# Kernel optimization log

Measured on AMD Instinct MI355X. Metric: run time of the kernel, lower is better.

The kernel has to match this reference:

```python
import jax, jax.numpy as jnp
import numpy as np

N_NODES = 100000
N_EDGES = 800000
IN_FEATS = 128
HIDDEN = 64
SCALE = 0.5 ** 0.5  # sqrt(0.5) residual scale
BN_EPS = 1e-5


def setup_inputs() -> dict:
    key = jax.random.key(0)
    ks = jax.random.split(key, 12)
    return {
        "src": jax.random.randint(ks[0], (N_EDGES,), 0, N_NODES, dtype=jnp.int64)
        if jax.config.jax_enable_x64 else jax.random.randint(ks[0], (N_EDGES,), 0, N_NODES),
        "dst": jax.random.randint(ks[1], (N_EDGES,), 0, N_NODES),
        "x": jax.random.normal(ks[2], (N_NODES, IN_FEATS), dtype=jnp.float32),
        "fc_w": jax.random.normal(ks[3], (IN_FEATS, HIDDEN), dtype=jnp.float32) * 0.05,
        "fc_b": jax.random.normal(ks[4], (HIDDEN,), dtype=jnp.float32) * 0.05,
        "w1": jax.random.normal(ks[5], (HIDDEN, HIDDEN), dtype=jnp.float32) * 0.05,
        "b1": jax.random.normal(ks[6], (HIDDEN,), dtype=jnp.float32) * 0.05,
        "w2": jax.random.normal(ks[7], (HIDDEN, HIDDEN), dtype=jnp.float32) * 0.05,
        "b2": jax.random.normal(ks[8], (HIDDEN,), dtype=jnp.float32) * 0.05,
        "gamma": jax.random.normal(ks[9], (HIDDEN,), dtype=jnp.float32) * 0.05 + 1.0,
        "beta": jax.random.normal(ks[10], (HIDDEN,), dtype=jnp.float32) * 0.05,
    }


def _graph_conv(h, w, b, src, dst, norm_src, norm_dst, n_nodes):
    # DGL GraphConv, norm='both': y = D_in^{-1/2} A D_out^{-1/2} (h W) + b
    h = h @ w                                   # [N, H]
    m = h[src] * norm_src[:, None]              # gather + src-degree norm, [E, H]
    agg = jax.ops.segment_sum(m, dst, num_segments=n_nodes)  # scatter-add, [N, H]
    return agg * norm_dst[:, None] + b


def reference(src, dst, x, fc_w, fc_b, w1, b1, w2, b2, gamma, beta):
    n_nodes = x.shape[0]
    ones_e = jnp.ones(src.shape[0], dtype=x.dtype)
    deg_out = jnp.clip(jax.ops.segment_sum(ones_e, src, num_segments=n_nodes), 1.0)
    deg_in = jnp.clip(jax.ops.segment_sum(ones_e, dst, num_segments=n_nodes), 1.0)
    norm_src = (deg_out ** -0.5)[src]           # per-edge source normalization
    norm_dst = deg_in ** -0.5                   # per-node destination normalization

    h = x @ fc_w + fc_b                          # fc: [N, H]
    h = (h + _graph_conv(h, w1, b1, src, dst, norm_src, norm_dst, n_nodes)) * SCALE
    h = (h + _graph_conv(h, w2, b2, src, dst, norm_src, norm_dst, n_nodes)) * SCALE

    # BatchNorm1d (training-mode batch statistics over nodes, biased variance)
    mu = h.mean(axis=0)
    var = ((h - mu) ** 2).mean(axis=0)
    h = (h - mu) * jax.lax.rsqrt(var + BN_EPS) * gamma + beta
    return h
```

## Files before the change

kernel.cpp:

```cpp
#include <hip/hip_runtime.h>

#define HIDDEN 64
#define INFEAT 128
#define SCALE_C 0.70710678118654752f
#define BN_EPS 1e-5f
#define AGG_GRID 2048
#define RED_BLK 32

__device__ __forceinline__ void hist_body(int bid, const int* __restrict__ src,
    const int* __restrict__ dst, int* __restrict__ degO, int* __restrict__ degI, int E){
  int e = bid * 256 + threadIdx.x;
  if (e < E){
    atomicAdd(&degO[src[e]], 1);
    atomicAdd(&degI[dst[e]], 1);
  }
}

__device__ __forceinline__ void place_body(int bid, const int* __restrict__ src,
    const int* __restrict__ dst, int* __restrict__ cur, int* __restrict__ cs, int E){
  int e = bid * 256 + threadIdx.x;
  if (e < E){
    int pos = atomicAdd(&cur[dst[e]], 1);
    cs[pos] = src[e];
  }
}

template<int KDIM, bool ADDB, bool SCALEROW>
__device__ __forceinline__ void gemm_body(int bid, const float* __restrict__ X,
    const float* __restrict__ W, const float* __restrict__ B,
    float* __restrict__ Y, const float* __restrict__ nrm, int N)
{
  __shared__ float xl[128 * 33];
  const int tid  = threadIdx.x;
  const int lane = tid & 63;
  const int wid  = __builtin_amdgcn_readfirstlane(tid >> 6);
  const int nodehalf = wid >> 1;
  const int c0 = (wid & 1) * 32;
  const int base = bid * 128;
  const int myNode = nodehalf * 64 + lane;
  const int gnode = base + myNode;

  float acc[32];
  #pragma unroll
  for (int c = 0; c < 32; ++c) acc[c] = ADDB ? B[c0 + c] : 0.f;

  constexpr int NCHUNK = KDIM / 32;
  #pragma unroll 1
  for (int ck = 0; ck < NCHUNK; ++ck){
    __syncthreads();
    #pragma unroll
    for (int i = 0; i < 4; ++i){
      int f  = i * 256 + tid;
      int nd = f >> 3;
      int kq = f & 7;
      float4 v = make_float4(0.f, 0.f, 0.f, 0.f);
      if (base + nd < N)
        v = *(const float4*)(X + (size_t)(base + nd) * KDIM + ck * 32 + kq * 4);
      float* p = &xl[nd * 33 + kq * 4];
      p[0] = v.x; p[1] = v.y; p[2] = v.z; p[3] = v.w;
    }
    __syncthreads();
    const float* wrow = W + (size_t)ck * 32 * HIDDEN + c0;
    #pragma unroll
    for (int k = 0; k < 32; ++k){
      float xv = xl[myNode * 33 + k];
      #pragma unroll
      for (int c = 0; c < 32; ++c)
        acc[c] = fmaf(xv, wrow[k * HIDDEN + c], acc[c]);
    }
  }

  if (gnode < N){
    float sc = SCALEROW ? nrm[gnode] : 1.f;
    float4* yp = (float4*)(Y + (size_t)gnode * HIDDEN + c0);
    #pragma unroll
    for (int j = 0; j < 8; ++j)
      yp[j] = make_float4(acc[4*j]*sc, acc[4*j+1]*sc, acc[4*j+2]*sc, acc[4*j+3]*sc);
  }
}

__device__ __forceinline__ int role_gemm_idx(int b, int GB, int TOT, int& histIdx){
  int fb  = (int)(((long)b * GB) / TOT);
  int fb1 = (int)(((long)(b + 1) * GB) / TOT);
  histIdx = b - fb;
  return (fb1 > fb) ? fb : -1;
}

__global__ __launch_bounds__(256) void k_mega1(const int* __restrict__ src,
    const int* __restrict__ dst, int* __restrict__ degO, int* __restrict__ degI, int E,
    const float* __restrict__ x, const float* __restrict__ fc_w,
    const float* __restrict__ fc_b, float* __restrict__ h, int N, int GB, int TOT){
  int hIdx;
  int g = role_gemm_idx(blockIdx.x, GB, TOT, hIdx);
  if (g >= 0) gemm_body<INFEAT, true, false>(g, x, fc_w, fc_b, h, nullptr, N);
  else        hist_body(hIdx, src, dst, degO, degI, E);
}

__global__ __launch_bounds__(256) void k_mega2(const int* __restrict__ src,
    const int* __restrict__ dst, int* __restrict__ cur, int* __restrict__ cs, int E,
    const float* __restrict__ h, const float* __restrict__ w1,
    float* __restrict__ t, const float* __restrict__ norm_out, int N, int GB, int TOT){
  int hIdx;
  int g = role_gemm_idx(blockIdx.x, GB, TOT, hIdx);
  if (g >= 0) gemm_body<HIDDEN, false, true>(g, h, w1, nullptr, t, norm_out, N);
  else        place_body(hIdx, src, dst, cur, cs, E);
}

__global__ __launch_bounds__(256) void k_gemm64(const float* __restrict__ X,
    const float* __restrict__ W, float* __restrict__ Y,
    const float* __restrict__ nrm, int N){
  gemm_body<HIDDEN, false, true>(blockIdx.x, X, W, nullptr, Y, nrm, N);
}

__global__ void k_scan1(const int* __restrict__ deg, int* __restrict__ bsum, int N){
  __shared__ int sh[256];
  int t = threadIdx.x;
  int i = blockIdx.x * 256 + t;
  sh[t] = (i < N) ? deg[i] : 0;
  __syncthreads();
  for (int ofs = 128; ofs > 0; ofs >>= 1){
    if (t < ofs) sh[t] += sh[t + ofs];
    __syncthreads();
  }
  if (t == 0) bsum[blockIdx.x] = sh[0];
}

__global__ void k_scan2(int* __restrict__ bsum, int NB){
  __shared__ int sh[512];
  int t = threadIdx.x;
  int v = (t < NB) ? bsum[t] : 0;
  sh[t] = v;
  __syncthreads();
  for (int ofs = 1; ofs < 512; ofs <<= 1){
    int u = (t >= ofs) ? sh[t - ofs] : 0;
    __syncthreads();
    sh[t] += u;
    __syncthreads();
  }
  if (t < NB) bsum[t] = sh[t] - v;
}

__global__ void k_scan3(const int* __restrict__ degI, const int* __restrict__ degO,
                        const int* __restrict__ bofs, int* __restrict__ rp,
                        int* __restrict__ cur, float* __restrict__ norm_out,
                        float* __restrict__ norm_in, int N, int E){
  __shared__ int sh[256];
  int t = threadIdx.x;
  int i = blockIdx.x * 256 + t;
  int v = (i < N) ? degI[i] : 0;
  sh[t] = v;
  __syncthreads();
  for (int ofs = 1; ofs < 256; ofs <<= 1){
    int u = (t >= ofs) ? sh[t - ofs] : 0;
    __syncthreads();
    sh[t] += u;
    __syncthreads();
  }
  if (i < N){
    int excl = sh[t] - v + bofs[blockIdx.x];
    rp[i] = excl; cur[i] = excl;
    if (i == N - 1) rp[N] = E;
    norm_out[i] = rsqrtf((float)max(degO[i], 1));
    norm_in[i]  = rsqrtf((float)max(v, 1));
  }
}

template<bool BN>
__global__ __launch_bounds__(256) void k_agg(const int* __restrict__ rp, const int* __restrict__ cs,
    const float* __restrict__ t, const float* __restrict__ norm_in,
    const float* __restrict__ b, float* __restrict__ h, float* __restrict__ bnpart, int N)
{
  const int tid = threadIdx.x;
  const int lane = tid & 63;
  const int wv = (blockIdx.x * 256 + tid) >> 6;
  const int nw = (gridDim.x * 256) >> 6;
  const float bv = b[lane];
  float s1 = 0.f, s2 = 0.f;

  for (int n = wv; n < N; n += nw){
    const int start = rp[n], end = rp[n + 1];
    float acc = 0.f;
    for (int j0 = start; j0 < end; j0 += 64){
      int cnt = end - j0; if (cnt > 64) cnt = 64;
      int sidx = (j0 + lane < end) ? cs[j0 + lane] : 0;
      int d = 0;
      for (; d + 4 <= cnt; d += 4){
        int a0 = __shfl(sidx, d),     a1 = __shfl(sidx, d + 1);
        int a2 = __shfl(sidx, d + 2), a3 = __shfl(sidx, d + 3);
        float v0 = t[(size_t)a0 * HIDDEN + lane];
        float v1 = t[(size_t)a1 * HIDDEN + lane];
        float v2 = t[(size_t)a2 * HIDDEN + lane];
        float v3 = t[(size_t)a3 * HIDDEN + lane];
        acc += v0; acc += v1; acc += v2; acc += v3;
      }
      for (; d < cnt; ++d){
        int a0 = __shfl(sidx, d);
        acc += t[(size_t)a0 * HIDDEN + lane];
      }
    }
    size_t idx = (size_t)n * HIDDEN + lane;
    float v = (h[idx] + acc * norm_in[n] + bv) * SCALE_C;
    h[idx] = v;
    if (BN){ s1 += v; s2 += v * v; }
  }

  if (BN){
    __shared__ float l1[256], l2[256];
    l1[tid] = s1; l2[tid] = s2;
    __syncthreads();
    if (tid < 64){
      float a1 = l1[tid] + l1[tid+64] + l1[tid+128] + l1[tid+192];
      float a2 = l2[tid] + l2[tid+64] + l2[tid+128] + l2[tid+192];
      bnpart[blockIdx.x * 128 + tid] = a1;
      bnpart[blockIdx.x * 128 + 64 + tid] = a2;
    }
  }
}

__global__ __launch_bounds__(256) void k_bnred(const float* __restrict__ bnpart,
    float* __restrict__ bnred, int nblk){
  int col  = threadIdx.x & 127;
  int half = threadIdx.x >> 7;
  int rows = nblk / RED_BLK;
  int r0 = blockIdx.x * rows;
  float s = 0.f;
  for (int r = half; r < rows; r += 2)
    s += bnpart[(size_t)(r0 + r) * 128 + col];
  __shared__ float sh[256];
  sh[threadIdx.x] = s;
  __syncthreads();
  if (threadIdx.x < 128)
    bnred[blockIdx.x * 128 + threadIdx.x] = sh[threadIdx.x] + sh[threadIdx.x + 128];
}

__global__ void k_bnfin(const float* __restrict__ bnred,
    const float* __restrict__ gamma, const float* __restrict__ beta,
    float* __restrict__ bnab, float invN){
  int c = threadIdx.x;
  float s1 = 0.f, s2 = 0.f;
  #pragma unroll
  for (int b = 0; b < RED_BLK; ++b){ s1 += bnred[b*128 + c]; s2 += bnred[b*128 + 64 + c]; }
  float mu  = s1 * invN;
  float var = s2 * invN - mu * mu;
  float rstd = rsqrtf(var + BN_EPS);
  float sc = gamma[c] * rstd;
  bnab[c] = sc;
  bnab[64 + c] = beta[c] - mu * sc;
}

__global__ void k_bnapply(float* __restrict__ h, const float* __restrict__ bnab, long total4){
  long i = (long)blockIdx.x * blockDim.x + threadIdx.x;
  if (i < total4){
    int c = (int)((i * 4) & 63);
    float4 v = ((float4*)h)[i];
    v.x = fmaf(v.x, bnab[c],     bnab[64 + c]);
    v.y = fmaf(v.y, bnab[c + 1], bnab[65 + c]);
    v.z = fmaf(v.z, bnab[c + 2], bnab[66 + c]);
    v.w = fmaf(v.w, bnab[c + 3], bnab[67 + c]);
    ((float4*)h)[i] = v;
  }
}

extern "C" void kernel_launch(void* const* d_in, const int* in_sizes, int n_in,
                              void* d_out, int out_size, void* d_ws, size_t ws_size,
                              hipStream_t stream){
  const int* src = (const int*)d_in[0];
  const int* dst = (const int*)d_in[1];
  const float* x     = (const float*)d_in[2];
  const float* fc_w  = (const float*)d_in[3];
  const float* fc_b  = (const float*)d_in[4];
  const float* w1    = (const float*)d_in[5];
  const float* b1    = (const float*)d_in[6];
  const float* w2    = (const float*)d_in[7];
  const float* b2    = (const float*)d_in[8];
  const float* gamma = (const float*)d_in[9];
  const float* beta  = (const float*)d_in[10];
  const int E = in_sizes[0];
  const int N = in_sizes[2] / INFEAT;
  const int NB = (N + 255) / 256;
  const int EB = (E + 255) / 256;
  const int GB = (N + 127) / 128;
  const int TOT = EB + GB;

  float* h = (float*)d_out;

  float* t        = (float*)d_ws;
  float* norm_out = t + (size_t)N * HIDDEN;
  float* norm_in  = norm_out + N;
  float* bnpart   = norm_in + N;
  float* bnred    = bnpart + AGG_GRID * 128;
  float* bnab     = bnred + RED_BLK * 128;
  int*   degO     = (int*)(bnab + 128);
  int*   degI     = degO + N;
  int*   rp       = degI + N;
  int*   cur      = rp + N + 1;
  int*   bsum     = cur + N;
  int*   cs       = bsum + 512;

  hipMemsetAsync(degO, 0, 2 * (size_t)N * sizeof(int), stream);

  k_mega1<<<TOT, 256, 0, stream>>>(src, dst, degO, degI, E,
                                   x, fc_w, fc_b, h, N, GB, TOT);

  k_scan1<<<NB, 256, 0, stream>>>(degI, bsum, N);
  k_scan2<<<1, 512, 0, stream>>>(bsum, NB);
  k_scan3<<<NB, 256, 0, stream>>>(degI, degO, bsum, rp, cur, norm_out, norm_in, N, E);

  k_mega2<<<TOT, 256, 0, stream>>>(src, dst, cur, cs, E,
                                   h, w1, t, norm_out, N, GB, TOT);

  k_agg<false><<<AGG_GRID, 256, 0, stream>>>(rp, cs, t, norm_in, b1, h, nullptr, N);

  k_gemm64<<<GB, 256, 0, stream>>>(h, w2, t, norm_out, N);
  k_agg<true><<<AGG_GRID, 256, 0, stream>>>(rp, cs, t, norm_in, b2, h, bnpart, N);

  k_bnred<<<RED_BLK, 256, 0, stream>>>(bnpart, bnred, AGG_GRID);
  k_bnfin<<<1, 64, 0, stream>>>(bnred, gamma, beta, bnab, 1.0f / (float)N);
  long total4 = (long)N * HIDDEN / 4;
  k_bnapply<<<(int)((total4 + 255) / 256), 256, 0, stream>>>(h, bnab, total4);
}
```

Before: 384.3 us.

## Fuse second GEMM into first aggregation epilogue using register-held W2

Folds the layer-2 feature transform (h @ w2 scaled by norm_out) into the layer-1 aggregation kernel. Each wavefront keeps its column of w2 in 64 registers and broadcasts the freshly computed row with readlane. This removes one kernel launch and one full re-read of h. The gather loop also switches from shfl to readlane and unrolls to 8 loads in flight. In exchange it adds register pressure that may lower occupancy of the latency-bound gather, and a second N×64 workspace buffer.

Result: slower. 410.7 us (+6.9%).

```diff
diff --git a/kernel.cpp b/kernel.cpp
--- a/kernel.cpp
+++ b/kernel.cpp
@@ -6,6 +6,11 @@
 #define BN_EPS 1e-5f
 #define AGG_GRID 2048
 #define RED_BLK 32
+
+__device__ __forceinline__ int rli(int v, int l){ return __builtin_amdgcn_readlane(v, l); }
+__device__ __forceinline__ float rlf(float v, int l){
+  return __uint_as_float(__builtin_amdgcn_readlane(__float_as_uint(v), l));
+}
 
 __device__ __forceinline__ void hist_body(int bid, const int* __restrict__ src,
     const int* __restrict__ dst, int* __restrict__ degO, int* __restrict__ degI, int E){
@@ -106,12 +111,6 @@
   else        place_body(hIdx, src, dst, cur, cs, E);
 }
 
-__global__ __launch_bounds__(256) void k_gemm64(const float* __restrict__ X,
-    const float* __restrict__ W, float* __restrict__ Y,
-    const float* __restrict__ nrm, int N){
-  gemm_body<HIDDEN, false, true>(blockIdx.x, X, W, nullptr, Y, nrm, N);
-}
-
 __global__ void k_scan1(const int* __restrict__ deg, int* __restrict__ bsum, int N){
   __shared__ int sh[256];
   int t = threadIdx.x;
@@ -165,10 +164,71 @@
   }
 }
 
-template<bool BN>
-__global__ __launch_bounds__(256) void k_agg(const int* __restrict__ rp, const int* __restrict__ cs,
-    const float* __restrict__ t, const float* __restrict__ norm_in,
-    const float* __restrict__ b, float* __restrict__ h, float* __restrict__ bnpart, int N)
+__device__ __forceinline__ float gather_row(const int* __restrict__ rp,
+    const int* __restrict__ cs, const float* __restrict__ t, int n, int lane){
+  const int start = rp[n], end = rp[n + 1];
+  float acc = 0.f;
+  for (int j0 = start; j0 < end; j0 += 64){
+    int cnt = end - j0; if (cnt > 64) cnt = 64;
+    int sidx = (j0 + lane < end) ? cs[j0 + lane] : 0;
+    int d = 0;
+    for (; d + 8 <= cnt; d += 8){
+      int a0 = rli(sidx, d),   a1 = rli(sidx, d+1);
+      int a2 = rli(sidx, d+2), a3 = rli(sidx, d+3);
+      int a4 = rli(sidx, d+4), a5 = rli(sidx, d+5);
+      int a6 = rli(sidx, d+6), a7 = rli(sidx, d+7);
+      float v0 = t[(size_t)a0 * HIDDEN + lane];
+      float v1 = t[(size_t)a1 * HIDDEN + lane];
+      float v2 = t[(size_t)a2 * HIDDEN + lane];
+      float v3 = t[(size_t)a3 * HIDDEN + lane];
+      float v4 = t[(size_t)a4 * HIDDEN + lane];
+      float v5 = t[(size_t)a5 * HIDDEN + lane];
+      float v6 = t[(size_t)a6 * HIDDEN + lane];
+      float v7 = t[(size_t)a7 * HIDDEN + lane];
+      acc += v0; acc += v1; acc += v2; acc += v3;
+      acc += v4; acc += v5; acc += v6; acc += v7;
+    }
+    for (; d < cnt; ++d)
+      acc += t[(size_t)rli(sidx, d) * HIDDEN + lane];
+  }
+  return acc;
+}
+
+__global__ __launch_bounds__(256) void k_aggmv(const int* __restrict__ rp,
+    const int* __restrict__ cs, const float* __restrict__ t1,
+    const float* __restrict__ norm_in, const float* __restrict__ norm_out,
+    const float* __restrict__ b, const float* __restrict__ w2,
+    float* __restrict__ h, float* __restrict__ t2, int N)
+{
+  const int tid = threadIdx.x;
+  const int lane = tid & 63;
+  const int wv = (blockIdx.x * 256 + tid) >> 6;
+  const int nw = (gridDim.x * 256) >> 6;
+  const float bv = b[lane];
+
+  float w2r[64];
+  #pragma unroll
+  for (int k = 0; k < 64; ++k) w2r[k] = w2[k * HIDDEN + lane];
+
+  for (int n = wv; n < N; n += nw){
+    float acc = gather_row(rp, cs, t1, n, lane);
+    size_t idx = (size_t)n * HIDDEN + lane;
+    float v = (h[idx] + acc * norm_in[n] + bv) * SCALE_C;
+    h[idx] = v;
+    float ta = 0.f, tb = 0.f;
+    #pragma unroll
+    for (int k = 0; k < 64; k += 2){
+      ta = fmaf(rlf(v, k),     w2r[k],     ta);
+      tb = fmaf(rlf(v, k + 1), w2r[k + 1], tb);
+    }
+    t2[idx] = (ta + tb) * norm_out[n];
+  }
+}
+
+__global__ __launch_bounds__(256) void k_agg2(const int* __restrict__ rp,
+    const int* __restrict__ cs, const float* __restrict__ t2,
+    const float* __restrict__ norm_in, const float* __restrict__ b,
+    float* __restrict__ h, float* __restrict__ bnpart, int N)
 {
   const int tid = threadIdx.x;
   const int lane = tid & 63;
@@ -178,42 +238,21 @@
   float s1 = 0.f, s2 = 0.f;
 
   for (int n = wv; n < N; n += nw){
-    const int start = rp[n], end = rp[n + 1];
-    float acc = 0.f;
-    for (int j0 = start; j0 < end; j0 += 64){
-      int cnt = end - j0; if (cnt > 64) cnt = 64;
-      int sidx = (j0 + lane < end) ? cs[j0 + lane] : 0;
-      int d = 0;
-      for (; d + 4 <= cnt; d += 4){
-        int a0 = __shfl(sidx, d),     a1 = __shfl(sidx, d + 1);
-        int a2 = __shfl(sidx, d + 2), a3 = __shfl(sidx, d + 3);
-        float v0 = t[(size_t)a0 * HIDDEN + lane];
-        float v1 = t[(size_t)a1 * HIDDEN + lane];
-        float v2 = t[(size_t)a2 * HIDDEN + lane];
-        float v3 = t[(size_t)a3 * HIDDEN + lane];
-        acc += v0; acc += v1; acc += v2; acc += v3;
-      }
-      for (; d < cnt; ++d){
-        int a0 = __shfl(sidx, d);
-        acc += t[(size_t)a0 * HIDDEN + lane];
-      }
-    }
+    float acc = gather_row(rp, cs, t2, n, lane);
     size_t idx = (size_t)n * HIDDEN + lane;
     float v = (h[idx] + acc * norm_in[n] + bv) * SCALE_C;
     h[idx] = v;
-    if (BN){ s1 += v; s2 += v * v; }
-  }
-
-  if (BN){
-    __shared__ float l1[256], l2[256];
-    l1[tid] = s1; l2[tid] = s2;
-    __syncthreads();
-    if (tid < 64){
-      float a1 = l1[tid] + l1[tid+64] + l1[tid+128] + l1[tid+192];
-      float a2 = l2[tid] + l2[tid+64] + l2[tid+128] + l2[tid+192];
-      bnpart[blockIdx.x * 128 + tid] = a1;
-      bnpart[blockIdx.x * 128 + 64 + tid] = a2;
-    }
+    s1 += v; s2 += v * v;
+  }
+
+  __shared__ float l1[256], l2[256];
+  l1[tid] = s1; l2[tid] = s2;
+  __syncthreads();
+  if (tid < 64){
+    float a1 = l1[tid] + l1[tid+64] + l1[tid+128] + l1[tid+192];
+    float a2 = l2[tid] + l2[tid+64] + l2[tid+128] + l2[tid+192];
+    bnpart[blockIdx.x * 128 + tid] = a1;
+    bnpart[blockIdx.x * 128 + 64 + tid] = a2;
   }
 }
 
@@ -284,8 +323,9 @@
 
   float* h = (float*)d_out;
 
-  float* t        = (float*)d_ws;
-  float* norm_out = t + (size_t)N * HIDDEN;
+  float* t1       = (float*)d_ws;
+  float* t2       = t1 + (size_t)N * HIDDEN;
+  float* norm_out = t2 + (size_t)N * HIDDEN;
   float* norm_in  = norm_out + N;
   float* bnpart   = norm_in + N;
   float* bnred    = bnpart + AGG_GRID * 128;
@@ -307,12 +347,11 @@
   k_scan3<<<NB, 256, 0, stream>>>(degI, degO, bsum, rp, cur, norm_out, norm_in, N, E);
 
   k_mega2<<<TOT, 256, 0, stream>>>(src, dst, cur, cs, E,
-                                   h, w1, t, norm_out, N, GB, TOT);
-
-  k_agg<false><<<AGG_GRID, 256, 0, stream>>>(rp, cs, t, norm_in, b1, h, nullptr, N);
-
-  k_gemm64<<<GB, 256, 0, stream>>>(h, w2, t, norm_out, N);
-  k_agg<true><<<AGG_GRID, 256, 0, stream>>>(rp, cs, t, norm_in, b2, h, bnpart, N);
+                                   h, w1, t1, norm_out, N, GB, TOT);
+
+  k_aggmv<<<AGG_GRID, 256, 0, stream>>>(rp, cs, t1, norm_in, norm_out, b1, w2, h, t2, N);
+
+  k_agg2<<<AGG_GRID, 256, 0, stream>>>(rp, cs, t2, norm_in, b2, h, bnpart, N);
 
   k_bnred<<<RED_BLK, 256, 0, stream>>>(bnpart, bnred, AGG_GRID);
   k_bnfin<<<1, 64, 0, stream>>>(bnred, gamma, beta, bnab, 1.0f / (float)N);
```

## Record edge ranks during histogram to drop placement atomics; use readlane in gather

Applied to the files above, without the earlier changes.

The in-degree histogram now stores each edge's atomicAdd return value as its rank within the destination's bucket. CSR placement then computes each slot directly as rp[dst]+rank, with no second round of atomics and no separate cursor array. The aggregation gather is moved into a helper that uses readlane instead of shuffle to broadcast source indices and unrolls 8 loads instead of 4. This adds an E-sized rank array to write and read back, and the readlane index must be wave-uniform, which holds here because d is uniform across the wave.

Measured after the change: 377.5 us. No clear change (-1.8%).

```diff
diff --git a/kernel.cpp b/kernel.cpp
--- a/kernel.cpp
+++ b/kernel.cpp
@@ -7,21 +7,24 @@
 #define AGG_GRID 2048
 #define RED_BLK 32
 
+__device__ __forceinline__ int rli(int v, int l){ return __builtin_amdgcn_readlane(v, l); }
+
 __device__ __forceinline__ void hist_body(int bid, const int* __restrict__ src,
-    const int* __restrict__ dst, int* __restrict__ degO, int* __restrict__ degI, int E){
+    const int* __restrict__ dst, int* __restrict__ degO, int* __restrict__ degI,
+    int* __restrict__ rank, int E){
   int e = bid * 256 + threadIdx.x;
   if (e < E){
     atomicAdd(&degO[src[e]], 1);
-    atomicAdd(&degI[dst[e]], 1);
+    rank[e] = atomicAdd(&degI[dst[e]], 1);
   }
 }
 
 __device__ __forceinline__ void place_body(int bid, const int* __restrict__ src,
-    const int* __restrict__ dst, int* __restrict__ cur, int* __restrict__ cs, int E){
+    const int* __restrict__ dst, const int* __restrict__ rank,
+    const int* __restrict__ rp, int* __restrict__ cs, int E){
   int e = bid * 256 + threadIdx.x;
   if (e < E){
-    int pos = atomicAdd(&cur[dst[e]], 1);
-    cs[pos] = src[e];
+    cs[rp[dst[e]] + rank[e]] = src[e];
   }
 }
 
@@ -87,23 +90,25 @@
 }
 
 __global__ __launch_bounds__(256) void k_mega1(const int* __restrict__ src,
-    const int* __restrict__ dst, int* __restrict__ degO, int* __restrict__ degI, int E,
+    const int* __restrict__ dst, int* __restrict__ degO, int* __restrict__ degI,
+    int* __restrict__ rank, int E,
     const float* __restrict__ x, const float* __restrict__ fc_w,
     const float* __restrict__ fc_b, float* __restrict__ h, int N, int GB, int TOT){
   int hIdx;
   int g = role_gemm_idx(blockIdx.x, GB, TOT, hIdx);
   if (g >= 0) gemm_body<INFEAT, true, false>(g, x, fc_w, fc_b, h, nullptr, N);
-  else        hist_body(hIdx, src, dst, degO, degI, E);
+  else        hist_body(hIdx, src, dst, degO, degI, rank, E);
 }
 
 __global__ __launch_bounds__(256) void k_mega2(const int* __restrict__ src,
-    const int* __restrict__ dst, int* __restrict__ cur, int* __restrict__ cs, int E,
+    const int* __restrict__ dst, const int* __restrict__ rank,
+    const int* __restrict__ rp, int* __restrict__ cs, int E,
     const float* __restrict__ h, const float* __restrict__ w1,
     float* __restrict__ t, const float* __restrict__ norm_out, int N, int GB, int TOT){
   int hIdx;
   int g = role_gemm_idx(blockIdx.x, GB, TOT, hIdx);
   if (g >= 0) gemm_body<HIDDEN, false, true>(g, h, w1, nullptr, t, norm_out, N);
-  else        place_body(hIdx, src, dst, cur, cs, E);
+  else        place_body(hIdx, src, dst, rank, rp, cs, E);
 }
 
 __global__ __launch_bounds__(256) void k_gemm64(const float* __restrict__ X,
@@ -142,8 +147,8 @@
 
 __global__ void k_scan3(const int* __restrict__ degI, const int* __restrict__ degO,
                         const int* __restrict__ bofs, int* __restrict__ rp,
-                        int* __restrict__ cur, float* __restrict__ norm_out,
-                        float* __restrict__ norm_in, int N, int E){
+                        float* __restrict__ norm_out, float* __restrict__ norm_in,
+                        int N, int E){
   __shared__ int sh[256];
   int t = threadIdx.x;
   int i = blockIdx.x * 256 + t;
@@ -158,11 +163,41 @@
   }
   if (i < N){
     int excl = sh[t] - v + bofs[blockIdx.x];
-    rp[i] = excl; cur[i] = excl;
+    rp[i] = excl;
     if (i == N - 1) rp[N] = E;
     norm_out[i] = rsqrtf((float)max(degO[i], 1));
     norm_in[i]  = rsqrtf((float)max(v, 1));
   }
+}
+
+__device__ __forceinline__ float gather_row(const int* __restrict__ rp,
+    const int* __restrict__ cs, const float* __restrict__ t, int n, int lane){
+  const int start = rp[n], end = rp[n + 1];
+  float acc = 0.f;
+  for (int j0 = start; j0 < end; j0 += 64){
+    int cnt = end - j0; if (cnt > 64) cnt = 64;
+    int sidx = (j0 + lane < end) ? cs[j0 + lane] : 0;
+    int d = 0;
+    for (; d + 8 <= cnt; d += 8){
+      int a0 = rli(sidx, d),   a1 = rli(sidx, d+1);
+      int a2 = rli(sidx, d+2), a3 = rli(sidx, d+3);
+      int a4 = rli(sidx, d+4), a5 = rli(sidx, d+5);
+      int a6 = rli(sidx, d+6), a7 = rli(sidx, d+7);
+      float v0 = t[(size_t)a0 * HIDDEN + lane];
+      float v1 = t[(size_t)a1 * HIDDEN + lane];
+      float v2 = t[(size_t)a2 * HIDDEN + lane];
+      float v3 = t[(size_t)a3 * HIDDEN + lane];
+      float v4 = t[(size_t)a4 * HIDDEN + lane];
+      float v5 = t[(size_t)a5 * HIDDEN + lane];
+      float v6 = t[(size_t)a6 * HIDDEN + lane];
+      float v7 = t[(size_t)a7 * HIDDEN + lane];
+      acc += v0; acc += v1; acc += v2; acc += v3;
+      acc += v4; acc += v5; acc += v6; acc += v7;
+    }
+    for (; d < cnt; ++d)
+      acc += t[(size_t)rli(sidx, d) * HIDDEN + lane];
+  }
+  return acc;
 }
 
 template<bool BN>
@@ -178,26 +213,7 @@
   float s1 = 0.f, s2 = 0.f;
 
   for (int n = wv; n < N; n += nw){
-    const int start = rp[n], end = rp[n + 1];
-    float acc = 0.f;
-    for (int j0 = start; j0 < end; j0 += 64){
-      int cnt = end - j0; if (cnt > 64) cnt = 64;
-      int sidx = (j0 + lane < end) ? cs[j0 + lane] : 0;
-      int d = 0;
-      for (; d + 4 <= cnt; d += 4){
-        int a0 = __shfl(sidx, d),     a1 = __shfl(sidx, d + 1);
-        int a2 = __shfl(sidx, d + 2), a3 = __shfl(sidx, d + 3);
-        float v0 = t[(size_t)a0 * HIDDEN + lane];
-        float v1 = t[(size_t)a1 * HIDDEN + lane];
-        float v2 = t[(size_t)a2 * HIDDEN + lane];
-        float v3 = t[(size_t)a3 * HIDDEN + lane];
-        acc += v0; acc += v1; acc += v2; acc += v3;
-      }
-      for (; d < cnt; ++d){
-        int a0 = __shfl(sidx, d);
-        acc += t[(size_t)a0 * HIDDEN + lane];
-      }
-    }
+    float acc = gather_row(rp, cs, t, n, lane);
     size_t idx = (size_t)n * HIDDEN + lane;
     float v = (h[idx] + acc * norm_in[n] + bv) * SCALE_C;
     h[idx] = v;
@@ -293,20 +309,20 @@
   int*   degO     = (int*)(bnab + 128);
   int*   degI     = degO + N;
   int*   rp       = degI + N;
-  int*   cur      = rp + N + 1;
-  int*   bsum     = cur + N;
-  int*   cs       = bsum + 512;
+  int*   bsum     = rp + N + 1;
+  int*   rank     = bsum + 512;
+  int*   cs       = rank + E;
 
   hipMemsetAsync(degO, 0, 2 * (size_t)N * sizeof(int), stream);
 
-  k_mega1<<<TOT, 256, 0, stream>>>(src, dst, degO, degI, E,
+  k_mega1<<<TOT, 256, 0, stream>>>(src, dst, degO, degI, rank, E,
                                    x, fc_w, fc_b, h, N, GB, TOT);
 
   k_scan1<<<NB, 256, 0, stream>>>(degI, bsum, N);
   k_scan2<<<1, 512, 0, stream>>>(bsum, NB);
-  k_scan3<<<NB, 256, 0, stream>>>(degI, degO, bsum, rp, cur, norm_out, norm_in, N, E);
-
-  k_mega2<<<TOT, 256, 0, stream>>>(src, dst, cur, cs, E,
+  k_scan3<<<NB, 256, 0, stream>>>(degI, degO, bsum, rp, norm_out, norm_in, N, E);
+
+  k_mega2<<<TOT, 256, 0, stream>>>(src, dst, rank, rp, cs, E,
                                    h, w1, t, norm_out, N, GB, TOT);
 
   k_agg<false><<<AGG_GRID, 256, 0, stream>>>(rp, cs, t, norm_in, b1, h, nullptr, N);
```
